# Optimization experiments

Hardware: AMD Instinct MI355X
Metric: run time of the kernel (lower is better)

The kernel has to match this reference:

```python
import jax, jax.numpy as jnp
import numpy as np

NEG_SLOPE = 0.01  # torch leaky_relu default

N_NODES = 100000
N_EDGES = 1600000
D = 64
N_BBOX = 4096


def setup_inputs() -> dict:
    key = jax.random.key(0)
    ks = jax.random.split(key, 9)
    x = jax.random.normal(ks[0], (N_NODES, D), dtype=jnp.float32)
    edge_index = jax.random.randint(ks[1], (2, N_EDGES), 0, N_NODES, dtype=jnp.int64)
    bbox = jax.random.randint(ks[2], (N_BBOX,), 0, N_NODES, dtype=jnp.int64)
    s = 1.0 / np.sqrt(D)
    W1_rel = jax.random.normal(ks[3], (D, D), dtype=jnp.float32) * s
    b1 = jax.random.normal(ks[4], (D,), dtype=jnp.float32) * s
    W1_root = jax.random.normal(ks[5], (D, D), dtype=jnp.float32) * s
    W2_rel = jax.random.normal(ks[6], (D, D), dtype=jnp.float32) * s
    b2 = jax.random.normal(ks[7], (D,), dtype=jnp.float32) * s
    W2_root = jax.random.normal(ks[8], (D, D), dtype=jnp.float32) * s
    return {"x": x, "edge_index": edge_index, "bbox": bbox,
            "W1_rel": W1_rel, "b1": b1, "W1_root": W1_root,
            "W2_rel": W2_rel, "b2": b2, "W2_root": W2_root}


def graph_conv(x, src, dst, W_rel, b, W_root):
    # PyG GraphConv: out_i = W_rel @ (sum_{j in N(i)} x_j) + b + W_root @ x_i
    msg = x[src]                                        # [E, D] gather
    agg = jax.ops.segment_sum(msg, dst, num_segments=x.shape[0])  # [N, D] scatter-add
    return agg @ W_rel + b + x @ W_root


def reference(x, edge_index, bbox, W1_rel, b1, W1_root, W2_rel, b2, W2_root):
    src, dst = edge_index[0], edge_index[1]
    h = graph_conv(x, src, dst, W1_rel, b1, W1_root)
    h = jax.nn.leaky_relu(h, NEG_SLOPE)
    # dropout is identity at inference (training=False)
    h = graph_conv(h, src, dst, W2_rel, b2, W2_root)
    h = jax.nn.leaky_relu(h, NEG_SLOPE)
    return h[bbox]
```

## Files before the change

### kernel.cpp

```cpp
#include <hip/hip_runtime.h>

#define N_NODES 100000
#define N_EDGES 1600000
#define D 64
#define N_BBOX 4096
#define CAP 64
#define NBITW 3136

__device__ __forceinline__ float readlane_f(float v, int l) {
  return __int_as_float(__builtin_amdgcn_readlane(__float_as_int(v), l));
}
__device__ __forceinline__ int bperm(int srclane, int v) {
  return __builtin_amdgcn_ds_bpermute(srclane << 2, v);
}
__device__ __forceinline__ float lrelu(float v) {
  return fmaxf(v, 0.01f * v);
}
__device__ __forceinline__ bool testbit(const unsigned* bits, int i) {
  return (bits[i >> 5] >> (i & 31)) & 1u;
}

__global__ __launch_bounds__(256) void mark_kernel(const int* __restrict__ bbox,
                                                   unsigned* __restrict__ is_bbox_bits,
                                                   unsigned* __restrict__ needed_bits) {
  int t = blockIdx.x * blockDim.x + threadIdx.x;
  if (t < N_BBOX) {
    int n = bbox[t];
    unsigned m = 1u << (n & 31);
    atomicOr(&is_bbox_bits[n >> 5], m);
    atomicOr(&needed_bits[n >> 5], m);
  }
}

__global__ __launch_bounds__(256) void mark_needed_kernel(
    const int* __restrict__ src, const int* __restrict__ dst,
    const unsigned* __restrict__ is_bbox_bits, unsigned* __restrict__ needed_bits) {
  int e = blockIdx.x * blockDim.x + threadIdx.x;
  if (e >= N_EDGES) return;
  int d = dst[e];
  if (testbit(is_bbox_bits, d)) {
    int s = src[e];
    atomicOr(&needed_bits[s >> 5], 1u << (s & 31));
  }
}

__global__ __launch_bounds__(256) void fill_kernel(const int* __restrict__ src,
                                                   const int* __restrict__ dst,
                                                   const unsigned* __restrict__ needed_bits,
                                                   int* __restrict__ cnt,
                                                   int* __restrict__ slots) {
  int e = blockIdx.x * blockDim.x + threadIdx.x;
  if (e >= N_EDGES) return;
  int d = dst[e];
  if (!testbit(needed_bits, d)) return;
  int p = atomicAdd(&cnt[d], 1);
  if (p < CAP) slots[(size_t)d * CAP + p] = src[e];
}

__global__ __launch_bounds__(256, 1) void layer1_fused_kernel(
    const float4* __restrict__ x4, const unsigned* __restrict__ needed_bits,
    const int* __restrict__ cnt, const int* __restrict__ slots,
    const float* __restrict__ W1rel, const float* __restrict__ b1,
    const float* __restrict__ W1root, float* __restrict__ hbuf) {
  const int lane = threadIdx.x & 63;
  const int wid0 = (blockIdx.x * blockDim.x + threadIdx.x) >> 6;
  const int nw = (gridDim.x * blockDim.x) >> 6;
  const int g = lane >> 4, c = lane & 15;

  float wrel[D], wroot[D];
#pragma unroll
  for (int k = 0; k < D; k++) {
    wrel[k] = W1rel[k * D + lane];
    wroot[k] = W1root[k * D + lane];
  }
  const float bj = b1[lane];

  for (int i = wid0; i < N_NODES; i += nw) {
    if (!testbit(needed_bits, i)) continue;
    int n = cnt[i];
    n = (n > CAP) ? CAP : n;
    const int myslot = (lane < n) ? slots[(size_t)i * CAP + lane] : 0;

    float4 acc = make_float4(0.f, 0.f, 0.f, 0.f);
    for (int e0 = 0; e0 < n; e0 += 16) {
      int idx[4], s[4];
      float4 v[4];
#pragma unroll
      for (int u = 0; u < 4; u++) {
        idx[u] = e0 + u * 4 + g;
        s[u] = bperm(idx[u], myslot);
      }
#pragma unroll
      for (int u = 0; u < 4; u++) {
        v[u] = make_float4(0.f, 0.f, 0.f, 0.f);
        if (idx[u] < n) v[u] = x4[(size_t)s[u] * 16 + c];
      }
#pragma unroll
      for (int u = 0; u < 4; u++) {
        acc.x += v[u].x; acc.y += v[u].y; acc.z += v[u].z; acc.w += v[u].w;
      }
    }
    acc.x += __shfl_xor(acc.x, 16); acc.y += __shfl_xor(acc.y, 16);
    acc.z += __shfl_xor(acc.z, 16); acc.w += __shfl_xor(acc.w, 16);
    acc.x += __shfl_xor(acc.x, 32); acc.y += __shfl_xor(acc.y, 32);
    acc.z += __shfl_xor(acc.z, 32); acc.w += __shfl_xor(acc.w, 32);

    const float xi = ((const float*)x4)[(size_t)i * D + lane];
    float s0 = 0.f, s1 = 0.f, s2 = 0.f, s3 = 0.f;
#pragma unroll
    for (int k = 0; k < D; k += 2) {
      const float a0 = (k & 2) ? readlane_f(acc.z, k >> 2) : readlane_f(acc.x, k >> 2);
      const float a1 = ((k + 1) & 2) ? readlane_f(acc.w, (k + 1) >> 2)
                                     : readlane_f(acc.y, (k + 1) >> 2);
      s0 += a0 * wrel[k];
      s1 += readlane_f(xi, k) * wroot[k];
      s2 += a1 * wrel[k + 1];
      s3 += readlane_f(xi, k + 1) * wroot[k + 1];
    }
    hbuf[(size_t)i * D + lane] = lrelu(bj + ((s0 + s1) + (s2 + s3)));
  }
}

__global__ __launch_bounds__(256, 1) void layer2_kernel(
    const float4* __restrict__ h4, const int* __restrict__ cnt,
    const int* __restrict__ slots, const int* __restrict__ bbox,
    const float* __restrict__ W2rel, const float* __restrict__ b2,
    const float* __restrict__ W2root, float* __restrict__ out) {
  const int t = (blockIdx.x * blockDim.x + threadIdx.x) >> 6;
  if (t >= N_BBOX) return;
  const int lane = threadIdx.x & 63;
  const int g = lane >> 4, c = lane & 15;

  float wrel[D], wroot[D];
#pragma unroll
  for (int k = 0; k < D; k++) {
    wrel[k] = W2rel[k * D + lane];
    wroot[k] = W2root[k * D + lane];
  }
  const float bj = b2[lane];

  const int node = __builtin_amdgcn_readfirstlane(bbox[t]);
  int n = cnt[node];
  n = (n > CAP) ? CAP : n;
  const int myslot = (lane < n) ? slots[(size_t)node * CAP + lane] : 0;

  float4 acc = make_float4(0.f, 0.f, 0.f, 0.f);
  for (int e0 = 0; e0 < n; e0 += 32) {
    int idx[8], s[8];
    float4 v[8];
#pragma unroll
    for (int u = 0; u < 8; u++) {
      idx[u] = e0 + u * 4 + g;
      s[u] = bperm(idx[u], myslot);
    }
#pragma unroll
    for (int u = 0; u < 8; u++) {
      v[u] = make_float4(0.f, 0.f, 0.f, 0.f);
      if (idx[u] < n) v[u] = h4[(size_t)s[u] * 16 + c];
    }
#pragma unroll
    for (int u = 0; u < 8; u++) {
      acc.x += v[u].x; acc.y += v[u].y; acc.z += v[u].z; acc.w += v[u].w;
    }
  }
  acc.x += __shfl_xor(acc.x, 16); acc.y += __shfl_xor(acc.y, 16);
  acc.z += __shfl_xor(acc.z, 16); acc.w += __shfl_xor(acc.w, 16);
  acc.x += __shfl_xor(acc.x, 32); acc.y += __shfl_xor(acc.y, 32);
  acc.z += __shfl_xor(acc.z, 32); acc.w += __shfl_xor(acc.w, 32);

  const float hi = ((const float*)h4)[(size_t)node * D + lane];
  float s0 = 0.f, s1 = 0.f, s2 = 0.f, s3 = 0.f;
#pragma unroll
  for (int k = 0; k < D; k += 2) {
    const float a0 = (k & 2) ? readlane_f(acc.z, k >> 2) : readlane_f(acc.x, k >> 2);
    const float a1 = ((k + 1) & 2) ? readlane_f(acc.w, (k + 1) >> 2)
                                   : readlane_f(acc.y, (k + 1) >> 2);
    s0 += a0 * wrel[k];
    s1 += readlane_f(hi, k) * wroot[k];
    s2 += a1 * wrel[k + 1];
    s3 += readlane_f(hi, k + 1) * wroot[k + 1];
  }
  out[(size_t)t * D + lane] = lrelu(bj + ((s0 + s1) + (s2 + s3)));
}


extern "C" void kernel_launch(void* const* d_in, const int* in_sizes, int n_in,
                              void* d_out, int out_size, void* d_ws, size_t ws_size,
                              hipStream_t stream) {
  const float* x = (const float*)d_in[0];
  const int* ei = (const int*)d_in[1];
  const int* src = ei;
  const int* dst = ei + N_EDGES;
  const int* bbox = (const int*)d_in[2];
  const float* W1rel = (const float*)d_in[3];
  const float* b1 = (const float*)d_in[4];
  const float* W1root = (const float*)d_in[5];
  const float* W2rel = (const float*)d_in[6];
  const float* b2 = (const float*)d_in[7];
  const float* W2root = (const float*)d_in[8];
  float* out = (float*)d_out;

  char* ws = (char*)d_ws;
  size_t off = 0;
  auto alloc = [&](size_t bytes) -> char* {
    char* p = ws + off;
    off = (off + bytes + 511) & ~(size_t)511;
    return p;
  };
  unsigned* is_bbox_bits = (unsigned*)alloc(NBITW * sizeof(unsigned));
  unsigned* needed_bits = (unsigned*)alloc(NBITW * sizeof(unsigned));
  int* cnt = (int*)alloc(N_NODES * sizeof(int));
  char* zero_end = ws + off;
  int* slots = (int*)alloc((size_t)N_NODES * CAP * sizeof(int));
  float* hbuf = (float*)alloc((size_t)N_NODES * D * sizeof(float));

  hipMemsetAsync(is_bbox_bits, 0, (size_t)(zero_end - (char*)is_bbox_bits), stream);
  mark_kernel<<<(N_BBOX + 255) / 256, 256, 0, stream>>>(bbox, is_bbox_bits,
                                                        needed_bits);
  mark_needed_kernel<<<(N_EDGES + 255) / 256, 256, 0, stream>>>(
      src, dst, is_bbox_bits, needed_bits);
  fill_kernel<<<(N_EDGES + 255) / 256, 256, 0, stream>>>(src, dst, needed_bits,
                                                         cnt, slots);
  layer1_fused_kernel<<<2048, 256, 0, stream>>>(
      (const float4*)x, needed_bits, cnt, slots, W1rel, b1, W1root, hbuf);
  layer2_kernel<<<(N_BBOX + 3) / 4, 256, 0, stream>>>(
      (const float4*)hbuf, cnt, slots, bbox, W2rel, b2, W2root, out);
}
```

Baseline: 226.4 us.

## Split layer-1 into neighbor gather and bf16 MFMA dense transform

The fused layer-1 kernel is split in two. A gather kernel sums neighbor features for each needed node into hbuf, with one wave per node and no weights held in registers. A dense kernel then computes agg@W_rel + x@W_root + b with LeakyReLU over all nodes in 16-row tiles, using bf16 MFMA 16x16x32 and writing back into hbuf in place. This replaces the register-heavy readlane scalar matmul and raises gather occupancy, at the cost of an extra round trip through memory, dense work on nodes that are not needed, and bf16 rounding of activations and weights.

```diff
diff --git a/kernel.cpp b/kernel.cpp
--- a/kernel.cpp
+++ b/kernel.cpp
@@ -7,6 +7,9 @@
 #define CAP 64
 #define NBITW 3136
 
+typedef short bf16x8 __attribute__((ext_vector_type(8)));
+typedef float f32x4 __attribute__((ext_vector_type(4)));
+
 __device__ __forceinline__ float readlane_f(float v, int l) {
   return __int_as_float(__builtin_amdgcn_readlane(__float_as_int(v), l));
 }
@@ -18,6 +21,17 @@
 }
 __device__ __forceinline__ bool testbit(const unsigned* bits, int i) {
   return (bits[i >> 5] >> (i & 31)) & 1u;
+}
+__device__ __forceinline__ short f2bf(float f) {
+  unsigned u = __float_as_uint(f);
+  u += 0x7FFFu + ((u >> 16) & 1u);
+  return (short)(u >> 16);
+}
+__device__ __forceinline__ bf16x8 pack_bf8(float4 lo, float4 hi) {
+  bf16x8 r;
+  r[0] = f2bf(lo.x); r[1] = f2bf(lo.y); r[2] = f2bf(lo.z); r[3] = f2bf(lo.w);
+  r[4] = f2bf(hi.x); r[5] = f2bf(hi.y); r[6] = f2bf(hi.z); r[7] = f2bf(hi.w);
+  return r;
 }
 
 __global__ __launch_bounds__(256) void mark_kernel(const int* __restrict__ bbox,
@@ -57,67 +71,103 @@
   if (p < CAP) slots[(size_t)d * CAP + p] = src[e];
 }
 
-__global__ __launch_bounds__(256, 1) void layer1_fused_kernel(
-    const float4* __restrict__ x4, const unsigned* __restrict__ needed_bits,
-    const int* __restrict__ cnt, const int* __restrict__ slots,
-    const float* __restrict__ W1rel, const float* __restrict__ b1,
-    const float* __restrict__ W1root, float* __restrict__ hbuf) {
+__global__ __launch_bounds__(256) void gather1_kernel(const float4* __restrict__ x4,
+                                                      const unsigned* __restrict__ needed_bits,
+                                                      const int* __restrict__ cnt,
+                                                      const int* __restrict__ slots,
+                                                      float4* __restrict__ agg4) {
+  const int wid = (blockIdx.x * blockDim.x + threadIdx.x) >> 6;
+  if (wid >= N_NODES) return;
+  if (!testbit(needed_bits, wid)) return;
   const int lane = threadIdx.x & 63;
+  const int g = lane >> 4, c = lane & 15;
+
+  int n = cnt[wid];
+  n = (n > CAP) ? CAP : n;
+  const int myslot = (lane < n) ? slots[(size_t)wid * CAP + lane] : 0;
+
+  float4 acc = make_float4(0.f, 0.f, 0.f, 0.f);
+  for (int e0 = 0; e0 < n; e0 += 32) {
+    int idx[8], s[8];
+    float4 v[8];
+#pragma unroll
+    for (int u = 0; u < 8; u++) {
+      idx[u] = e0 + u * 4 + g;
+      s[u] = bperm(idx[u], myslot);
+    }
+#pragma unroll
+    for (int u = 0; u < 8; u++) {
+      v[u] = make_float4(0.f, 0.f, 0.f, 0.f);
+      if (idx[u] < n) v[u] = x4[(size_t)s[u] * 16 + c];
+    }
+#pragma unroll
+    for (int u = 0; u < 8; u++) {
+      acc.x += v[u].x; acc.y += v[u].y; acc.z += v[u].z; acc.w += v[u].w;
+    }
+  }
+  acc.x += __shfl_xor(acc.x, 16); acc.y += __shfl_xor(acc.y, 16);
+  acc.z += __shfl_xor(acc.z, 16); acc.w += __shfl_xor(acc.w, 16);
+  acc.x += __shfl_xor(acc.x, 32); acc.y += __shfl_xor(acc.y, 32);
+  acc.z += __shfl_xor(acc.z, 32); acc.w += __shfl_xor(acc.w, 32);
+  if (g == 0) agg4[(size_t)wid * 16 + c] = acc;
+}
+
+__global__ __launch_bounds__(256, 1) void dense1_mfma_kernel(
+    const float* __restrict__ x, const float* __restrict__ W1rel,
+    const float* __restrict__ b1, const float* __restrict__ W1root,
+    float* __restrict__ hbuf) {
+  const int lane = threadIdx.x & 63;
+  const int cn = lane & 15;
+  const int quad = lane >> 4;
   const int wid0 = (blockIdx.x * blockDim.x + threadIdx.x) >> 6;
-  const int nw = (gridDim.x * blockDim.x) >> 6;
-  const int g = lane >> 4, c = lane & 15;
-
-  float wrel[D], wroot[D];
-#pragma unroll
-  for (int k = 0; k < D; k++) {
-    wrel[k] = W1rel[k * D + lane];
-    wroot[k] = W1root[k * D + lane];
-  }
-  const float bj = b1[lane];
-
-  for (int i = wid0; i < N_NODES; i += nw) {
-    if (!testbit(needed_bits, i)) continue;
-    int n = cnt[i];
-    n = (n > CAP) ? CAP : n;
-    const int myslot = (lane < n) ? slots[(size_t)i * CAP + lane] : 0;
-
-    float4 acc = make_float4(0.f, 0.f, 0.f, 0.f);
-    for (int e0 = 0; e0 < n; e0 += 16) {
-      int idx[4], s[4];
-      float4 v[4];
-#pragma unroll
-      for (int u = 0; u < 4; u++) {
-        idx[u] = e0 + u * 4 + g;
-        s[u] = bperm(idx[u], myslot);
+  const int nwaves = (gridDim.x * blockDim.x) >> 6;
+
+  bf16x8 brel[2][4], broot[2][4];
+#pragma unroll
+  for (int kh = 0; kh < 2; kh++)
+#pragma unroll
+    for (int nt = 0; nt < 4; nt++)
+#pragma unroll
+      for (int i = 0; i < 8; i++) {
+        const int k = kh * 32 + quad * 8 + i;
+        brel[kh][nt][i] = f2bf(W1rel[k * D + nt * 16 + cn]);
+        broot[kh][nt][i] = f2bf(W1root[k * D + nt * 16 + cn]);
       }
-#pragma unroll
-      for (int u = 0; u < 4; u++) {
-        v[u] = make_float4(0.f, 0.f, 0.f, 0.f);
-        if (idx[u] < n) v[u] = x4[(size_t)s[u] * 16 + c];
+  float bj[4];
+#pragma unroll
+  for (int nt = 0; nt < 4; nt++) bj[nt] = b1[nt * 16 + cn];
+
+  for (int tile = wid0; tile < N_NODES / 16; tile += nwaves) {
+    const int node0 = tile * 16;
+    const float* arow = hbuf + (size_t)(node0 + cn) * D;
+    const float* xrow = x + (size_t)(node0 + cn) * D;
+
+    f32x4 acc[4] = {};
+#pragma unroll
+    for (int kh = 0; kh < 2; kh++) {
+      const int kb = kh * 32 + quad * 8;
+      const float4 fa0 = *(const float4*)(arow + kb);
+      const float4 fa1 = *(const float4*)(arow + kb + 4);
+      const float4 fx0 = *(const float4*)(xrow + kb);
+      const float4 fx1 = *(const float4*)(xrow + kb + 4);
+      const bf16x8 a_agg = pack_bf8(fa0, fa1);
+      const bf16x8 a_x = pack_bf8(fx0, fx1);
+#pragma unroll
+      for (int nt = 0; nt < 4; nt++) {
+        acc[nt] = __builtin_amdgcn_mfma_f32_16x16x32_bf16(a_agg, brel[kh][nt],
+                                                          acc[nt], 0, 0, 0);
+        acc[nt] = __builtin_amdgcn_mfma_f32_16x16x32_bf16(a_x, broot[kh][nt],
+                                                          acc[nt], 0, 0, 0);
       }
-#pragma unroll
-      for (int u = 0; u < 4; u++) {
-        acc.x += v[u].x; acc.y += v[u].y; acc.z += v[u].z; acc.w += v[u].w;
+    }
+#pragma unroll
+    for (int nt = 0; nt < 4; nt++) {
+#pragma unroll
+      for (int r = 0; r < 4; r++) {
+        const int row = quad * 4 + r;
+        hbuf[(size_t)(node0 + row) * D + nt * 16 + cn] = lrelu(acc[nt][r] + bj[nt]);
       }
     }
-    acc.x += __shfl_xor(acc.x, 16); acc.y += __shfl_xor(acc.y, 16);
-    acc.z += __shfl_xor(acc.z, 16); acc.w += __shfl_xor(acc.w, 16);
-    acc.x += __shfl_xor(acc.x, 32); acc.y += __shfl_xor(acc.y, 32);
-    acc.z += __shfl_xor(acc.z, 32); acc.w += __shfl_xor(acc.w, 32);
-
-    const float xi = ((const float*)x4)[(size_t)i * D + lane];
-    float s0 = 0.f, s1 = 0.f, s2 = 0.f, s3 = 0.f;
-#pragma unroll
-    for (int k = 0; k < D; k += 2) {
-      const float a0 = (k & 2) ? readlane_f(acc.z, k >> 2) : readlane_f(acc.x, k >> 2);
-      const float a1 = ((k + 1) & 2) ? readlane_f(acc.w, (k + 1) >> 2)
-                                     : readlane_f(acc.y, (k + 1) >> 2);
-      s0 += a0 * wrel[k];
-      s1 += readlane_f(xi, k) * wroot[k];
-      s2 += a1 * wrel[k + 1];
-      s3 += readlane_f(xi, k + 1) * wroot[k + 1];
-    }
-    hbuf[(size_t)i * D + lane] = lrelu(bj + ((s0 + s1) + (s2 + s3)));
   }
 }
 
@@ -221,8 +271,9 @@
       src, dst, is_bbox_bits, needed_bits);
   fill_kernel<<<(N_EDGES + 255) / 256, 256, 0, stream>>>(src, dst, needed_bits,
                                                          cnt, slots);
-  layer1_fused_kernel<<<2048, 256, 0, stream>>>(
-      (const float4*)x, needed_bits, cnt, slots, W1rel, b1, W1root, hbuf);
+  gather1_kernel<<<(N_NODES + 3) / 4, 256, 0, stream>>>(
+      (const float4*)x, needed_bits, cnt, slots, (float4*)hbuf);
+  dense1_mfma_kernel<<<512, 256, 0, stream>>>(x, W1rel, b1, W1root, hbuf);
   layer2_kernel<<<(N_BBOX + 3) / 4, 256, 0, stream>>>(
       (const float4*)hbuf, cnt, slots, bbox, W2rel, b2, W2root, out);
 }
```

Measured after the change: 201.7 us. 10.9% less time.
